# Performance work log

Measured on AMD Instinct MI355X. Metric: run time of the kernel, lower is better.

Reference implementation:

```python
import jax, jax.numpy as jnp
import numpy as np

N = 100000          # nodes
E = 1600000         # edges
IN_F = 128          # in_features
OUT_F = 64          # attention_dim = out_features
H = 8               # heads
D_K = OUT_F // H    # 8


def setup_inputs() -> dict:
    key = jax.random.key(0)
    ks = jax.random.split(key, 8)
    x = jax.random.normal(ks[0], (N, IN_F), dtype=jnp.float32)
    edge = jax.random.randint(ks[1], (2, E), 0, N, dtype=jnp.int64)
    # Linear weights stored torch-style [out, in]; biases [out].
    Wq = jax.random.normal(ks[2], (OUT_F, IN_F), dtype=jnp.float32) * 0.02
    bq = jax.random.normal(ks[3], (OUT_F,), dtype=jnp.float32) * 0.02
    Wk = jax.random.normal(ks[4], (OUT_F, IN_F), dtype=jnp.float32) * 0.02
    bk = jax.random.normal(ks[5], (OUT_F,), dtype=jnp.float32) * 0.02
    Wv = jax.random.normal(ks[6], (OUT_F, IN_F), dtype=jnp.float32) * 0.02
    bv = jax.random.normal(ks[7], (OUT_F,), dtype=jnp.float32) * 0.02
    return {"x": x, "edge": edge, "Wq": Wq, "bq": bq, "Wk": Wk, "bk": bk, "Wv": Wv, "bv": bv}


def _segment_softmax(scores, seg_ids, num_segments):
    # scores: [E, H], seg_ids: [E]; stable softmax grouped by seg_ids
    seg_max = jax.ops.segment_max(scores, seg_ids, num_segments=num_segments)  # [N, H]
    seg_max = jnp.where(jnp.isfinite(seg_max), seg_max, 0.0)
    ex = jnp.exp(scores - seg_max[seg_ids])                                    # [E, H]
    denom = jax.ops.segment_sum(ex, seg_ids, num_segments=num_segments)        # [N, H]
    return ex / (denom[seg_ids] + 1e-16)


def reference(x, edge, Wq, bq, Wk, bk, Wv, bv):
    src_idx = edge[0]  # source node per edge (softmax group + output row)
    dst_idx = edge[1]  # destination node per edge (k/v gather)

    q = (x @ Wq.T + bq).reshape(N, H, D_K)  # [N, H, D_K]
    k = (x @ Wk.T + bk).reshape(N, H, D_K)
    v = (x @ Wv.T + bv).reshape(N, H, D_K)

    # per-edge dot-product attention scores over d_k
    prods = jnp.sum(q[src_idx] * k[dst_idx], axis=-1) / np.sqrt(D_K)  # [E, H]
    attn = _segment_softmax(prods, src_idx, N)                         # [E, H]

    # spmm per head, vectorized: out[i] = sum_{e: src=i} attn[e,h] * v[dst[e],h,:]
    msgs = attn[:, :, None] * v[dst_idx]                               # [E, H, D_K]
    out = jax.ops.segment_sum(msgs, src_idx, num_segments=N)           # [N, H, D_K]
    # head-major concat matches torch loop-concat of [N, D_K] blocks
    return out.reshape(N, H * D_K)
```

## Files before the change

### kernel.cpp

```cpp
#include <hip/hip_runtime.h>

#define N_NODES   100000
#define E_EDGES   1600000
#define IN_FEATS  128
#define OUT_FEATS 64
#define NH        8
#define DK        8

#define QKV_BLOCKS 782
#define E4         (E_EDGES / 4)

#define REGIONS    196
#define RCAP       8960
#define SC_BLOCKS  391
#define RC_STRIDE  16

typedef __attribute__((ext_vector_type(8))) short short8;
typedef __attribute__((ext_vector_type(4))) float floatx4;

__device__ __forceinline__ ushort f2bf(float f) {
    uint u = __float_as_uint(f);
    u += 0x7FFF + ((u >> 16) & 1);
    return (ushort)(u >> 16);
}
__device__ __forceinline__ float bflo(uint u) { return __uint_as_float(u << 16); }
__device__ __forceinline__ float bfhi(uint u) { return __uint_as_float(u & 0xFFFF0000u); }

__global__ __launch_bounds__(256) void prep_kernel(
    const float* __restrict__ Wq, const float* __restrict__ Wk,
    const float* __restrict__ Wv, ushort* __restrict__ Wb,
    uint* __restrict__ rcount)
{
    const int i = blockIdx.x * 256 + threadIdx.x;
    if (i < REGIONS * RC_STRIDE) rcount[i] = 0;
    if (i < 3072) {
        const int m  = i >> 10;
        const int kc = (i >> 8) & 3;
        const int qd = (i >> 6) & 3;
        const int nt = (i >> 4) & 3;
        const int lm = i & 15;
        const float* W = (m == 0) ? Wq : (m == 1) ? Wk : Wv;
        const float* s = W + (16 * nt + lm) * IN_FEATS + 32 * kc + 8 * qd;
        const float4 f0 = ((const float4*)s)[0];
        const float4 f1 = ((const float4*)s)[1];
        ushort r[8];
        r[0] = f2bf(f0.x); r[1] = f2bf(f0.y); r[2] = f2bf(f0.z); r[3] = f2bf(f0.w);
        r[4] = f2bf(f1.x); r[5] = f2bf(f1.y); r[6] = f2bf(f1.z); r[7] = f2bf(f1.w);
        const int di = (kc >> 1) * 1536 + m * 512 + (kc & 1) * 256 + qd * 64 + nt * 16 + lm;
        *(short8*)(Wb + (size_t)di * 8) = *(short8*)r;
    }
}

__global__ __launch_bounds__(512) void scatter_kernel(
    const int* __restrict__ src, const int* __restrict__ dst,
    uint* __restrict__ rcount, uint* __restrict__ seg)
{
    __shared__ uint hist[REGIONS];
    __shared__ uint gbase[REGIONS];

    const int tid = threadIdx.x;
    const int gt  = blockIdx.x * 512 + tid;

    if (tid < REGIONS) hist[tid] = 0;
    __syncthreads();

    int sv[8], dv[8], loc[8];
    int nv = 0;
    #pragma unroll
    for (int p = 0; p < 2; ++p) {
        const int qi = gt * 2 + p;
        if (qi < E4) {
            const int4 s4 = ((const int4*)src)[qi];
            const int4 d4 = ((const int4*)dst)[qi];
            sv[p * 4 + 0] = s4.x; sv[p * 4 + 1] = s4.y;
            sv[p * 4 + 2] = s4.z; sv[p * 4 + 3] = s4.w;
            dv[p * 4 + 0] = d4.x; dv[p * 4 + 1] = d4.y;
            dv[p * 4 + 2] = d4.z; dv[p * 4 + 3] = d4.w;
            nv = p * 4 + 4;
        }
    }

    #pragma unroll
    for (int e = 0; e < 8; ++e) {
        if (e < nv) loc[e] = (int)atomicAdd(&hist[sv[e] >> 9], 1u);
    }
    __syncthreads();

    if (tid < REGIONS) {
        const uint h = hist[tid];
        gbase[tid] = h ? atomicAdd(&rcount[tid * RC_STRIDE], h) : 0u;
    }
    __syncthreads();

    #pragma unroll
    for (int e = 0; e < 8; ++e) {
        if (e < nv) {
            const int  r   = sv[e] >> 9;
            const uint pos = gbase[r] + (uint)loc[e];
            if (pos < RCAP)
                seg[(size_t)r * RCAP + pos] =
                    (uint)dv[e] | ((uint)(sv[e] & 511) << 17);
        }
    }
}

__global__ __launch_bounds__(512) void build_kernel(
    const uint* __restrict__ rcount, const uint* __restrict__ seg,
    uint* __restrict__ dense, int* __restrict__ node_off,
    int* __restrict__ degw)
{
    __shared__ uint ec[RCAP];
    __shared__ uint cnt[512];
    __shared__ uint cnt2[512];
    __shared__ uint off[512];
    __shared__ uint wsum[8];

    const int r    = blockIdx.x;
    const int tid  = threadIdx.x;
    const int lane = tid & 63;
    const int wid  = tid >> 6;
    const int n0   = r << 9;

    int m = (int)rcount[r * RC_STRIDE];
    if (m > RCAP) m = RCAP;

    cnt[tid]  = 0;
    cnt2[tid] = 0;
    for (int i = tid; i < m; i += 512) ec[i] = seg[(size_t)r * RCAP + i];
    __syncthreads();

    for (int i = tid; i < m; i += 512) atomicAdd(&cnt[ec[i] >> 17], 1u);
    __syncthreads();

    const uint v = cnt[tid];
    uint inc = v;
    #pragma unroll
    for (int d = 1; d < 64; d <<= 1) {
        const uint t = __shfl_up(inc, d);
        if (lane >= d) inc += t;
    }
    if (lane == 63) wsum[wid] = inc;
    __syncthreads();
    if (tid == 0) {
        uint a = 0;
        #pragma unroll
        for (int w2 = 0; w2 < 8; ++w2) { const uint t = wsum[w2]; wsum[w2] = a; a += t; }
    }
    __syncthreads();
    off[tid] = inc - v + wsum[wid];
    __syncthreads();

    for (int i = tid; i < m; i += 512) {
        const uint s = ec[i] >> 17;
        const uint p = off[s] + atomicAdd(&cnt2[s], 1u);
        dense[(size_t)r * RCAP + p] = ec[i] & 0x1FFFFu;
    }

    const int node = n0 + tid;
    if (node < N_NODES) {
        node_off[node] = r * RCAP + (int)off[tid];
        degw[node]     = (int)cnt[tid];
    }
}

__global__ __launch_bounds__(512) void qkv_kernel(
    const float* __restrict__ x, const ushort* __restrict__ Wb,
    const float* __restrict__ bq, const float* __restrict__ bk,
    const float* __restrict__ bv,
    float* __restrict__ qo, uint* __restrict__ kvo)
{
    __shared__ short8 wlds[1536];

    const int t    = threadIdx.x;
    const int lane = t & 63;
    const int w    = t >> 6;
    const int lm   = lane & 15;
    const int qd   = lane >> 4;
    const int row0 = blockIdx.x * 128 + 16 * w;

    #pragma unroll
    for (int c = 0; c < 3; ++c) {
        const int i = t + 512 * c;
        wlds[i] = *(const short8*)(Wb + (size_t)i * 8);
    }

    const int  arow   = row0 + lm;
    const bool avalid = arow < N_NODES;
    short8 afrag[4];
    #pragma unroll
    for (int kc = 0; kc < 4; ++kc) {
        float4 f0 = make_float4(0.f, 0.f, 0.f, 0.f);
        float4 f1 = f0;
        if (avalid) {
            const float4* xp =
                (const float4*)(x + (size_t)arow * IN_FEATS + kc * 32 + qd * 8);
            f0 = xp[0];
            f1 = xp[1];
        }
        short8 a;
        a[0] = (short)f2bf(f0.x); a[1] = (short)f2bf(f0.y);
        a[2] = (short)f2bf(f0.z); a[3] = (short)f2bf(f0.w);
        a[4] = (short)f2bf(f1.x); a[5] = (short)f2bf(f1.y);
        a[6] = (short)f2bf(f1.z); a[7] = (short)f2bf(f1.w);
        afrag[kc] = a;
    }

    floatx4 qacc[4], kacc[4], vacc[4];
    #pragma unroll
    for (int nt = 0; nt < 4; ++nt) {
        const float bbq = bq[16 * nt + lm];
        const float bbk = bk[16 * nt + lm];
        const float bbv = bv[16 * nt + lm];
        qacc[nt] = (floatx4){bbq, bbq, bbq, bbq};
        kacc[nt] = (floatx4){bbk, bbk, bbk, bbk};
        vacc[nt] = (floatx4){bbv, bbv, bbv, bbv};
    }

    __syncthreads();

    #pragma unroll
    for (int kc = 0; kc < 2; ++kc) {
        const int fb = (kc & 1) * 256 + qd * 64 + lm;
        #pragma unroll
        for (int nt = 0; nt < 4; ++nt) {
            const short8 bq8 = wlds[fb + nt * 16];
            const short8 bk8 = wlds[fb + nt * 16 + 512];
            const short8 bv8 = wlds[fb + nt * 16 + 1024];
            qacc[nt] = __builtin_amdgcn_mfma_f32_16x16x32_bf16(afrag[kc], bq8, qacc[nt], 0, 0, 0);
            kacc[nt] = __builtin_amdgcn_mfma_f32_16x16x32_bf16(afrag[kc], bk8, kacc[nt], 0, 0, 0);
            vacc[nt] = __builtin_amdgcn_mfma_f32_16x16x32_bf16(afrag[kc], bv8, vacc[nt], 0, 0, 0);
        }
    }

    __syncthreads();

    #pragma unroll
    for (int c = 0; c < 3; ++c) {
        const int i = t + 512 * c;
        wlds[i] = *(const short8*)(Wb + (size_t)(1536 + i) * 8);
    }

    __syncthreads();

    #pragma unroll
    for (int kc = 2; kc < 4; ++kc) {
        const int fb = (kc & 1) * 256 + qd * 64 + lm;
        #pragma unroll
        for (int nt = 0; nt < 4; ++nt) {
            const short8 bq8 = wlds[fb + nt * 16];
            const short8 bk8 = wlds[fb + nt * 16 + 512];
            const short8 bv8 = wlds[fb + nt * 16 + 1024];
            qacc[nt] = __builtin_amdgcn_mfma_f32_16x16x32_bf16(afrag[kc], bq8, qacc[nt], 0, 0, 0);
            kacc[nt] = __builtin_amdgcn_mfma_f32_16x16x32_bf16(afrag[kc], bk8, kacc[nt], 0, 0, 0);
            vacc[nt] = __builtin_amdgcn_mfma_f32_16x16x32_bf16(afrag[kc], bv8, vacc[nt], 0, 0, 0);
        }
    }

    #pragma unroll
    for (int nt = 0; nt < 4; ++nt) {
        #pragma unroll
        for (int reg = 0; reg < 4; ++reg) {
            const int row = row0 + 4 * qd + reg;
            if (row < N_NODES) {
                qo[(size_t)row * OUT_FEATS + 16 * nt + lm] = qacc[nt][reg];
                const uint kb = f2bf(kacc[nt][reg]);
                const uint vb = f2bf(vacc[nt][reg]);
                kvo[(size_t)row * OUT_FEATS + 16 * nt + lm] = kb | (vb << 16);
            }
        }
    }
}

__global__ __launch_bounds__(256) void attn_kernel(
    const float* __restrict__ q, const uint* __restrict__ kv,
    const uint* __restrict__ dense, const int* __restrict__ node_off,
    const int* __restrict__ degw, float* __restrict__ out)
{
    const int lane = threadIdx.x & 63;
    const int wv   = threadIdx.x >> 6;
    const int node = blockIdx.x * 4 + wv;
    const int h    = lane >> 3;
    const int jme  = lane & 7;

    const float4* qrow = (const float4*)(q + (size_t)node * OUT_FEATS + h * DK);
    const float4 qa = qrow[0];
    const float4 qb = qrow[1];

    const int offn = node_off[node];
    int deg = degw[node];
    deg = deg < 64 ? deg : 64;

    int dn_lane = 0;
    if (lane < deg) dn_lane = (int)dense[(size_t)offn + lane];

    float den = 0.f;
    float a0 = 0.f, a1 = 0.f, a2 = 0.f, a3 = 0.f;
    float a4 = 0.f, a5 = 0.f, a6 = 0.f, a7 = 0.f;

    int g = 0;
    for (; g + 16 <= deg; g += 16) {
        const int dnA = __shfl(dn_lane, g + jme);
        const int dnB = __shfl(dn_lane, g + 8 + jme);
        const uint4* kpA = (const uint4*)(kv + (size_t)dnA * OUT_FEATS + h * DK);
        const uint4* kpB = (const uint4*)(kv + (size_t)dnB * OUT_FEATS + h * DK);
        const uint4 uaA = kpA[0];
        const uint4 ubA = kpA[1];
        const uint4 uaB = kpB[0];
        const uint4 ubB = kpB[1];

        float pA = qa.x * bflo(uaA.x) + qa.y * bflo(uaA.y) +
                   qa.z * bflo(uaA.z) + qa.w * bflo(uaA.w) +
                   qb.x * bflo(ubA.x) + qb.y * bflo(ubA.y) +
                   qb.z * bflo(ubA.z) + qb.w * bflo(ubA.w);
        float pB = qa.x * bflo(uaB.x) + qa.y * bflo(uaB.y) +
                   qa.z * bflo(uaB.z) + qa.w * bflo(uaB.w) +
                   qb.x * bflo(ubB.x) + qb.y * bflo(ubB.y) +
                   qb.z * bflo(ubB.z) + qb.w * bflo(ubB.w);
        const float exA = exp2f(pA * 0.51006971413f);
        const float exB = exp2f(pB * 0.51006971413f);

        den += exA;
        a0 += exA * bfhi(uaA.x); a1 += exA * bfhi(uaA.y);
        a2 += exA * bfhi(uaA.z); a3 += exA * bfhi(uaA.w);
        a4 += exA * bfhi(ubA.x); a5 += exA * bfhi(ubA.y);
        a6 += exA * bfhi(ubA.z); a7 += exA * bfhi(ubA.w);
        den += exB;
        a0 += exB * bfhi(uaB.x); a1 += exB * bfhi(uaB.y);
        a2 += exB * bfhi(uaB.z); a3 += exB * bfhi(uaB.w);
        a4 += exB * bfhi(ubB.x); a5 += exB * bfhi(ubB.y);
        a6 += exB * bfhi(ubB.z); a7 += exB * bfhi(ubB.w);
    }
    for (; g < deg; g += 8) {
        const int dn = __shfl(dn_lane, g + jme);
        const uint4* kvp = (const uint4*)(kv + (size_t)dn * OUT_FEATS + h * DK);
        const uint4 ua = kvp[0];
        const uint4 ub = kvp[1];

        float p = qa.x * bflo(ua.x) + qa.y * bflo(ua.y) +
                  qa.z * bflo(ua.z) + qa.w * bflo(ua.w) +
                  qb.x * bflo(ub.x) + qb.y * bflo(ub.y) +
                  qb.z * bflo(ub.z) + qb.w * bflo(ub.w);
        float ex = exp2f(p * 0.51006971413f);
        if (g + jme >= deg) ex = 0.f;

        den += ex;
        a0 += ex * bfhi(ua.x); a1 += ex * bfhi(ua.y);
        a2 += ex * bfhi(ua.z); a3 += ex * bfhi(ua.w);
        a4 += ex * bfhi(ub.x); a5 += ex * bfhi(ub.y);
        a6 += ex * bfhi(ub.z); a7 += ex * bfhi(ub.w);
    }

    #pragma unroll
    for (int m = 1; m <= 4; m <<= 1) {
        den += __shfl_xor(den, m);
        a0 += __shfl_xor(a0, m); a1 += __shfl_xor(a1, m);
        a2 += __shfl_xor(a2, m); a3 += __shfl_xor(a3, m);
        a4 += __shfl_xor(a4, m); a5 += __shfl_xor(a5, m);
        a6 += __shfl_xor(a6, m); a7 += __shfl_xor(a7, m);
    }

    float r = a0;
    r = (jme == 1) ? a1 : r;
    r = (jme == 2) ? a2 : r;
    r = (jme == 3) ? a3 : r;
    r = (jme == 4) ? a4 : r;
    r = (jme == 5) ? a5 : r;
    r = (jme == 6) ? a6 : r;
    r = (jme == 7) ? a7 : r;

    out[(size_t)node * OUT_FEATS + lane] = r / (den + 1e-16f);
}

extern "C" void kernel_launch(void* const* d_in, const int* in_sizes, int n_in,
                              void* d_out, int out_size, void* d_ws, size_t ws_size,
                              hipStream_t stream)
{
    const float* x  = (const float*)d_in[0];
    const int*  edge = (const int*)d_in[1];
    const float* Wq = (const float*)d_in[2];
    const float* bq = (const float*)d_in[3];
    const float* Wk = (const float*)d_in[4];
    const float* bk = (const float*)d_in[5];
    const float* Wv = (const float*)d_in[6];
    const float* bv = (const float*)d_in[7];
    float* out = (float*)d_out;

    float*  q        = (float*)d_ws;
    uint*   kv       = (uint*)(q + (size_t)N_NODES * OUT_FEATS);
    ushort* Wb       = (ushort*)(kv + (size_t)N_NODES * OUT_FEATS);
    uint*   rcount   = (uint*)(Wb + 3 * 64 * IN_FEATS);
    uint*   seg      = rcount + REGIONS * RC_STRIDE;
    uint*   dense    = seg + (size_t)REGIONS * RCAP;
    int*    node_off = (int*)(dense + (size_t)REGIONS * RCAP);
    int*    degw     = node_off + N_NODES;

    const int* src = edge;
    const int* dst = edge + E_EDGES;

    prep_kernel<<<13, 256, 0, stream>>>(Wq, Wk, Wv, Wb, rcount);

    scatter_kernel<<<SC_BLOCKS, 512, 0, stream>>>(src, dst, rcount, seg);

    build_kernel<<<REGIONS, 512, 0, stream>>>(rcount, seg, dense, node_off, degw);

    qkv_kernel<<<QKV_BLOCKS, 512, 0, stream>>>(x, Wb, bq, bk, bv, q, kv);

    attn_kernel<<<N_NODES / 4, 256, 0, stream>>>(q, kv, dense, node_off, degw, out);
}
```

Measured before the change: 216.8 us.

## Fuse QKV projection and edge scatter into one interleaved launch

Merges the independent edge-scatter and QKV projection kernels into a single launch. Every third block does scatter work and the others do the MFMA projection, so memory- and atomic-bound scatter work can overlap with compute-bound projection work. This removes one kernel launch and its tail. In exchange, scatter blocks reserve the larger shared-memory footprint, and the build kernel now runs after both finish.

After: 209.2 us. 3.5% less time.

```diff
diff --git a/kernel.cpp b/kernel.cpp
--- a/kernel.cpp
+++ b/kernel.cpp
@@ -14,6 +14,7 @@
 #define RCAP       8960
 #define SC_BLOCKS  391
 #define RC_STRIDE  16
+#define FUSED_BLOCKS (QKV_BLOCKS + SC_BLOCKS)
 
 typedef __attribute__((ext_vector_type(8))) short short8;
 typedef __attribute__((ext_vector_type(4))) float floatx4;
@@ -51,55 +52,166 @@
     }
 }
 
-__global__ __launch_bounds__(512) void scatter_kernel(
+__global__ __launch_bounds__(512) void qkv_scatter_kernel(
+    const float* __restrict__ x, const ushort* __restrict__ Wb,
+    const float* __restrict__ bq, const float* __restrict__ bk,
+    const float* __restrict__ bv,
+    float* __restrict__ qo, uint* __restrict__ kvo,
     const int* __restrict__ src, const int* __restrict__ dst,
     uint* __restrict__ rcount, uint* __restrict__ seg)
 {
+    __shared__ short8 wlds[1536];
     __shared__ uint hist[REGIONS];
     __shared__ uint gbase[REGIONS];
 
+    const int b   = blockIdx.x;
+    const int bm  = b % 3;
     const int tid = threadIdx.x;
-    const int gt  = blockIdx.x * 512 + tid;
-
-    if (tid < REGIONS) hist[tid] = 0;
-    __syncthreads();
-
-    int sv[8], dv[8], loc[8];
-    int nv = 0;
-    #pragma unroll
-    for (int p = 0; p < 2; ++p) {
-        const int qi = gt * 2 + p;
-        if (qi < E4) {
-            const int4 s4 = ((const int4*)src)[qi];
-            const int4 d4 = ((const int4*)dst)[qi];
-            sv[p * 4 + 0] = s4.x; sv[p * 4 + 1] = s4.y;
-            sv[p * 4 + 2] = s4.z; sv[p * 4 + 3] = s4.w;
-            dv[p * 4 + 0] = d4.x; dv[p * 4 + 1] = d4.y;
-            dv[p * 4 + 2] = d4.z; dv[p * 4 + 3] = d4.w;
-            nv = p * 4 + 4;
-        }
-    }
-
-    #pragma unroll
-    for (int e = 0; e < 8; ++e) {
-        if (e < nv) loc[e] = (int)atomicAdd(&hist[sv[e] >> 9], 1u);
-    }
-    __syncthreads();
-
-    if (tid < REGIONS) {
-        const uint h = hist[tid];
-        gbase[tid] = h ? atomicAdd(&rcount[tid * RC_STRIDE], h) : 0u;
-    }
-    __syncthreads();
-
-    #pragma unroll
-    for (int e = 0; e < 8; ++e) {
-        if (e < nv) {
-            const int  r   = sv[e] >> 9;
-            const uint pos = gbase[r] + (uint)loc[e];
-            if (pos < RCAP)
-                seg[(size_t)r * RCAP + pos] =
-                    (uint)dv[e] | ((uint)(sv[e] & 511) << 17);
+
+    if (bm == 2) {
+        const int sc = b / 3;
+        const int gt = sc * 512 + tid;
+
+        if (tid < REGIONS) hist[tid] = 0;
+        __syncthreads();
+
+        int sv[8], dv[8], loc[8];
+        int nv = 0;
+        #pragma unroll
+        for (int p = 0; p < 2; ++p) {
+            const int qi = gt * 2 + p;
+            if (qi < E4) {
+                const int4 s4 = ((const int4*)src)[qi];
+                const int4 d4 = ((const int4*)dst)[qi];
+                sv[p * 4 + 0] = s4.x; sv[p * 4 + 1] = s4.y;
+                sv[p * 4 + 2] = s4.z; sv[p * 4 + 3] = s4.w;
+                dv[p * 4 + 0] = d4.x; dv[p * 4 + 1] = d4.y;
+                dv[p * 4 + 2] = d4.z; dv[p * 4 + 3] = d4.w;
+                nv = p * 4 + 4;
+            }
+        }
+
+        #pragma unroll
+        for (int e = 0; e < 8; ++e) {
+            if (e < nv) loc[e] = (int)atomicAdd(&hist[sv[e] >> 9], 1u);
+        }
+        __syncthreads();
+
+        if (tid < REGIONS) {
+            const uint h = hist[tid];
+            gbase[tid] = h ? atomicAdd(&rcount[tid * RC_STRIDE], h) : 0u;
+        }
+        __syncthreads();
+
+        #pragma unroll
+        for (int e = 0; e < 8; ++e) {
+            if (e < nv) {
+                const int  r   = sv[e] >> 9;
+                const uint pos = gbase[r] + (uint)loc[e];
+                if (pos < RCAP)
+                    seg[(size_t)r * RCAP + pos] =
+                        (uint)dv[e] | ((uint)(sv[e] & 511) << 17);
+            }
+        }
+        return;
+    }
+
+    const int qb   = (b / 3) * 2 + bm;
+    const int lane = tid & 63;
+    const int w    = tid >> 6;
+    const int lm   = lane & 15;
+    const int qd   = lane >> 4;
+    const int row0 = qb * 128 + 16 * w;
+
+    #pragma unroll
+    for (int c = 0; c < 3; ++c) {
+        const int i = tid + 512 * c;
+        wlds[i] = *(const short8*)(Wb + (size_t)i * 8);
+    }
+
+    const int  arow   = row0 + lm;
+    const bool avalid = arow < N_NODES;
+    short8 afrag[4];
+    #pragma unroll
+    for (int kc = 0; kc < 4; ++kc) {
+        float4 f0 = make_float4(0.f, 0.f, 0.f, 0.f);
+        float4 f1 = f0;
+        if (avalid) {
+            const float4* xp =
+                (const float4*)(x + (size_t)arow * IN_FEATS + kc * 32 + qd * 8);
+            f0 = xp[0];
+            f1 = xp[1];
+        }
+        short8 a;
+        a[0] = (short)f2bf(f0.x); a[1] = (short)f2bf(f0.y);
+        a[2] = (short)f2bf(f0.z); a[3] = (short)f2bf(f0.w);
+        a[4] = (short)f2bf(f1.x); a[5] = (short)f2bf(f1.y);
+        a[6] = (short)f2bf(f1.z); a[7] = (short)f2bf(f1.w);
+        afrag[kc] = a;
+    }
+
+    floatx4 qacc[4], kacc[4], vacc[4];
+    #pragma unroll
+    for (int nt = 0; nt < 4; ++nt) {
+        const float bbq = bq[16 * nt + lm];
+        const float bbk = bk[16 * nt + lm];
+        const float bbv = bv[16 * nt + lm];
+        qacc[nt] = (floatx4){bbq, bbq, bbq, bbq};
+        kacc[nt] = (floatx4){bbk, bbk, bbk, bbk};
+        vacc[nt] = (floatx4){bbv, bbv, bbv, bbv};
+    }
+
+    __syncthreads();
+
+    #pragma unroll
+    for (int kc = 0; kc < 2; ++kc) {
+        const int fb = (kc & 1) * 256 + qd * 64 + lm;
+        #pragma unroll
+        for (int nt = 0; nt < 4; ++nt) {
+            const short8 bq8 = wlds[fb + nt * 16];
+            const short8 bk8 = wlds[fb + nt * 16 + 512];
+            const short8 bv8 = wlds[fb + nt * 16 + 1024];
+            qacc[nt] = __builtin_amdgcn_mfma_f32_16x16x32_bf16(afrag[kc], bq8, qacc[nt], 0, 0, 0);
+            kacc[nt] = __builtin_amdgcn_mfma_f32_16x16x32_bf16(afrag[kc], bk8, kacc[nt], 0, 0, 0);
+            vacc[nt] = __builtin_amdgcn_mfma_f32_16x16x32_bf16(afrag[kc], bv8, vacc[nt], 0, 0, 0);
+        }
+    }
+
+    __syncthreads();
+
+    #pragma unroll
+    for (int c = 0; c < 3; ++c) {
+        const int i = tid + 512 * c;
+        wlds[i] = *(const short8*)(Wb + (size_t)(1536 + i) * 8);
+    }
+
+    __syncthreads();
+
+    #pragma unroll
+    for (int kc = 2; kc < 4; ++kc) {
+        const int fb = (kc & 1) * 256 + qd * 64 + lm;
+        #pragma unroll
+        for (int nt = 0; nt < 4; ++nt) {
+            const short8 bq8 = wlds[fb + nt * 16];
+            const short8 bk8 = wlds[fb + nt * 16 + 512];
+            const short8 bv8 = wlds[fb + nt * 16 + 1024];
+            qacc[nt] = __builtin_amdgcn_mfma_f32_16x16x32_bf16(afrag[kc], bq8, qacc[nt], 0, 0, 0);
+            kacc[nt] = __builtin_amdgcn_mfma_f32_16x16x32_bf16(afrag[kc], bk8, kacc[nt], 0, 0, 0);
+            vacc[nt] = __builtin_amdgcn_mfma_f32_16x16x32_bf16(afrag[kc], bv8, vacc[nt], 0, 0, 0);
+        }
+    }
+
+    #pragma unroll
+    for (int nt = 0; nt < 4; ++nt) {
+        #pragma unroll
+        for (int reg = 0; reg < 4; ++reg) {
+            const int row = row0 + 4 * qd + reg;
+            if (row < N_NODES) {
+                qo[(size_t)row * OUT_FEATS + 16 * nt + lm] = qacc[nt][reg];
+                const uint kb = f2bf(kacc[nt][reg]);
+                const uint vb = f2bf(vacc[nt][reg]);
+                kvo[(size_t)row * OUT_FEATS + 16 * nt + lm] = kb | (vb << 16);
+            }
         }
     }
 }
@@ -160,114 +272,6 @@
     if (node < N_NODES) {
         node_off[node] = r * RCAP + (int)off[tid];
         degw[node]     = (int)cnt[tid];
-    }
-}
-
-__global__ __launch_bounds__(512) void qkv_kernel(
-    const float* __restrict__ x, const ushort* __restrict__ Wb,
-    const float* __restrict__ bq, const float* __restrict__ bk,
-    const float* __restrict__ bv,
-    float* __restrict__ qo, uint* __restrict__ kvo)
-{
-    __shared__ short8 wlds[1536];
-
-    const int t    = threadIdx.x;
-    const int lane = t & 63;
-    const int w    = t >> 6;
-    const int lm   = lane & 15;
-    const int qd   = lane >> 4;
-    const int row0 = blockIdx.x * 128 + 16 * w;
-
-    #pragma unroll
-    for (int c = 0; c < 3; ++c) {
-        const int i = t + 512 * c;
-        wlds[i] = *(const short8*)(Wb + (size_t)i * 8);
-    }
-
-    const int  arow   = row0 + lm;
-    const bool avalid = arow < N_NODES;
-    short8 afrag[4];
-    #pragma unroll
-    for (int kc = 0; kc < 4; ++kc) {
-        float4 f0 = make_float4(0.f, 0.f, 0.f, 0.f);
-        float4 f1 = f0;
-        if (avalid) {
-            const float4* xp =
-                (const float4*)(x + (size_t)arow * IN_FEATS + kc * 32 + qd * 8);
-            f0 = xp[0];
-            f1 = xp[1];
-        }
-        short8 a;
-        a[0] = (short)f2bf(f0.x); a[1] = (short)f2bf(f0.y);
-        a[2] = (short)f2bf(f0.z); a[3] = (short)f2bf(f0.w);
-        a[4] = (short)f2bf(f1.x); a[5] = (short)f2bf(f1.y);
-        a[6] = (short)f2bf(f1.z); a[7] = (short)f2bf(f1.w);
-        afrag[kc] = a;
-    }
-
-    floatx4 qacc[4], kacc[4], vacc[4];
-    #pragma unroll
-    for (int nt = 0; nt < 4; ++nt) {
-        const float bbq = bq[16 * nt + lm];
-        const float bbk = bk[16 * nt + lm];
-        const float bbv = bv[16 * nt + lm];
-        qacc[nt] = (floatx4){bbq, bbq, bbq, bbq};
-        kacc[nt] = (floatx4){bbk, bbk, bbk, bbk};
-        vacc[nt] = (floatx4){bbv, bbv, bbv, bbv};
-    }
-
-    __syncthreads();
-
-    #pragma unroll
-    for (int kc = 0; kc < 2; ++kc) {
-        const int fb = (kc & 1) * 256 + qd * 64 + lm;
-        #pragma unroll
-        for (int nt = 0; nt < 4; ++nt) {
-            const short8 bq8 = wlds[fb + nt * 16];
-            const short8 bk8 = wlds[fb + nt * 16 + 512];
-            const short8 bv8 = wlds[fb + nt * 16 + 1024];
-            qacc[nt] = __builtin_amdgcn_mfma_f32_16x16x32_bf16(afrag[kc], bq8, qacc[nt], 0, 0, 0);
-            kacc[nt] = __builtin_amdgcn_mfma_f32_16x16x32_bf16(afrag[kc], bk8, kacc[nt], 0, 0, 0);
-            vacc[nt] = __builtin_amdgcn_mfma_f32_16x16x32_bf16(afrag[kc], bv8, vacc[nt], 0, 0, 0);
-        }
-    }
-
-    __syncthreads();
-
-    #pragma unroll
-    for (int c = 0; c < 3; ++c) {
-        const int i = t + 512 * c;
-        wlds[i] = *(const short8*)(Wb + (size_t)(1536 + i) * 8);
-    }
-
-    __syncthreads();
-
-    #pragma unroll
-    for (int kc = 2; kc < 4; ++kc) {
-        const int fb = (kc & 1) * 256 + qd * 64 + lm;
-        #pragma unroll
-        for (int nt = 0; nt < 4; ++nt) {
-            const short8 bq8 = wlds[fb + nt * 16];
-            const short8 bk8 = wlds[fb + nt * 16 + 512];
-            const short8 bv8 = wlds[fb + nt * 16 + 1024];
-            qacc[nt] = __builtin_amdgcn_mfma_f32_16x16x32_bf16(afrag[kc], bq8, qacc[nt], 0, 0, 0);
-            kacc[nt] = __builtin_amdgcn_mfma_f32_16x16x32_bf16(afrag[kc], bk8, kacc[nt], 0, 0, 0);
-            vacc[nt] = __builtin_amdgcn_mfma_f32_16x16x32_bf16(afrag[kc], bv8, vacc[nt], 0, 0, 0);
-        }
-    }
-
-    #pragma unroll
-    for (int nt = 0; nt < 4; ++nt) {
-        #pragma unroll
-        for (int reg = 0; reg < 4; ++reg) {
-            const int row = row0 + 4 * qd + reg;
-            if (row < N_NODES) {
-                qo[(size_t)row * OUT_FEATS + 16 * nt + lm] = qacc[nt][reg];
-                const uint kb = f2bf(kacc[nt][reg]);
-                const uint vb = f2bf(vacc[nt][reg]);
-                kvo[(size_t)row * OUT_FEATS + 16 * nt + lm] = kb | (vb << 16);
-            }
-        }
     }
 }
 
@@ -399,11 +403,10 @@
 
     prep_kernel<<<13, 256, 0, stream>>>(Wq, Wk, Wv, Wb, rcount);
 
-    scatter_kernel<<<SC_BLOCKS, 512, 0, stream>>>(src, dst, rcount, seg);
+    qkv_scatter_kernel<<<FUSED_BLOCKS, 512, 0, stream>>>(
+        x, Wb, bq, bk, bv, q, kv, src, dst, rcount, seg);
 
     build_kernel<<<REGIONS, 512, 0, stream>>>(rcount, seg, dense, node_off, degw);
 
-    qkv_kernel<<<QKV_BLOCKS, 512, 0, stream>>>(x, Wb, bq, bk, bv, q, kv);
-
     attn_kernel<<<N_NODES / 4, 256, 0, stream>>>(q, kv, dense, node_off, degw, out);
 }
```
